# Kernel optimization log

Hardware: AMD Instinct MI355X
Metric: run time of the kernel (lower is better)

The kernel has to match this reference:

```python
import jax, jax.numpy as jnp
import numpy as np

B, S, V, K = 8, 128, 32000, 32


def setup_inputs() -> dict:
    key = jax.random.key(0)
    ks = jax.random.split(key, 8)
    return {
        "neural_logit": jax.random.normal(ks[0], (B, S, V), dtype=jnp.float32),
        "optor_vals": jax.random.randint(ks[1], (B, S, K), 0, V),
        "optor_dists": jax.random.uniform(ks[2], (B, S, K), dtype=jnp.float32) * 100.0,
        "const_vals": jax.random.randint(ks[3], (B, S, K), 0, V),
        "const_dists": jax.random.uniform(ks[4], (B, S, K), dtype=jnp.float32) * 100.0,
        "prev_words": jax.random.randint(ks[5], (B, S), 0, V),
        "optor_lamda": jnp.array([0.7], dtype=jnp.float32),
        "const_lamda": jnp.array([0.7], dtype=jnp.float32),
        "optor_temp": jnp.array([10.0], dtype=jnp.float32),
        "const_temp": jnp.array([10.0], dtype=jnp.float32),
    }


def _knn_prob(vals, dists, temp, vocab):
    # kernel-density: softmax over negative distances, scatter-add into vocab ids
    b, s, k = vals.shape
    w = jax.nn.softmax(-dists / temp, axis=-1)            # [B,S,K]
    rows = jnp.arange(b * s)[:, None]                     # [BS,1]
    p = jnp.zeros((b * s, vocab), w.dtype)
    p = p.at[rows, vals.reshape(b * s, k)].add(w.reshape(b * s, k))
    return p.reshape(b, s, vocab)


def reference(neural_logit, optor_vals, optor_dists, const_vals, const_dists,
              prev_words, optor_lamda, const_lamda, optor_temp, const_temp):
    nmt_prob = jax.nn.softmax(neural_logit, axis=-1)      # [B,S,V]

    optor_knn = _knn_prob(optor_vals, optor_dists, optor_temp[0], V)
    optor_combined = optor_lamda[0] * optor_knn + (1.0 - optor_lamda[0]) * nmt_prob

    const_knn = _knn_prob(const_vals, const_dists, const_temp[0], V)
    const_combined = const_lamda[0] * const_knn + (1.0 - const_lamda[0]) * nmt_prob

    pw = prev_words                                        # [B,S]
    optor_mask = (pw <= 88) | ((pw >= 91) & (pw <= 291))
    const_mask = (pw == 89) | (pw == 90) | (pw >= 292)

    combined = (optor_combined * optor_mask[:, :, None].astype(nmt_prob.dtype)
                + const_combined * const_mask[:, :, None].astype(nmt_prob.dtype))
    return combined
```

## Files before the change

### kernel.cpp

```cpp
#include <hip/hip_runtime.h>
#include <math.h>

constexpr int Bc = 8, Sc = 128, Vc = 32000, Kc = 32;
constexpr int NT = 1024;
constexpr int V4 = Vc / 4;
constexpr int ITERS = (V4 + NT - 1) / NT;
constexpr int NWAVES = NT / 64;

__global__ __launch_bounds__(NT) void SR_knnModel_kernel(
    const float* __restrict__ logit,
    const int*   __restrict__ optor_vals,
    const float* __restrict__ optor_dists,
    const int*   __restrict__ const_vals,
    const float* __restrict__ const_dists,
    const int*   __restrict__ prev_words,
    const float* __restrict__ optor_lamda,
    const float* __restrict__ const_lamda,
    const float* __restrict__ optor_temp,
    const float* __restrict__ const_temp,
    float* __restrict__ out)
{
    const int row = blockIdx.x;
    const int t   = threadIdx.x;
    const size_t base = (size_t)row * Vc;
    const float4* __restrict__ xin  = (const float4*)(logit + base);
    float4* __restrict__       xout = (float4*)(out + base);

    float4 r[ITERS];
    float lmax = -INFINITY;
#pragma unroll
    for (int i = 0; i < ITERS; ++i) {
        const int idx = t + i * NT;
        if (i < ITERS - 1 || idx < V4) {
            const float4 v = xin[idx];
            r[i] = v;
            lmax = fmaxf(lmax, fmaxf(fmaxf(v.x, v.y), fmaxf(v.z, v.w)));
        }
    }

    __shared__ float red[NWAVES];
#pragma unroll
    for (int off = 32; off > 0; off >>= 1)
        lmax = fmaxf(lmax, __shfl_xor(lmax, off));
    const int wave = t >> 6;
    if ((t & 63) == 0) red[wave] = lmax;
    __syncthreads();
    float bmax = red[0];
#pragma unroll
    for (int w = 1; w < NWAVES; ++w) bmax = fmaxf(bmax, red[w]);
    __syncthreads();

    float lsum = 0.f;
#pragma unroll
    for (int i = 0; i < ITERS; ++i) {
        const int idx = t + i * NT;
        if (i < ITERS - 1 || idx < V4) {
            float4 v = r[i];
            v.x = __expf(v.x - bmax);
            v.y = __expf(v.y - bmax);
            v.z = __expf(v.z - bmax);
            v.w = __expf(v.w - bmax);
            r[i] = v;
            lsum += (v.x + v.y) + (v.z + v.w);
        }
    }
#pragma unroll
    for (int off = 32; off > 0; off >>= 1)
        lsum += __shfl_xor(lsum, off);
    if ((t & 63) == 0) red[wave] = lsum;
    __syncthreads();
    float bsum = 0.f;
#pragma unroll
    for (int w = 0; w < NWAVES; ++w) bsum += red[w];

    const int pw = prev_words[row];
    const bool om = (pw <= 88) || (pw >= 91 && pw <= 291);
    const bool cm = (pw == 89) || (pw == 90) || (pw >= 292);
    const float omf = om ? 1.f : 0.f;
    const float cmf = cm ? 1.f : 0.f;
    const float ol = optor_lamda[0];
    const float cl = const_lamda[0];
    const float cn = (1.f - ol) * omf + (1.f - cl) * cmf;
    const float inv = cn / bsum;

#pragma unroll
    for (int i = 0; i < ITERS; ++i) {
        const int idx = t + i * NT;
        if (i < ITERS - 1 || idx < V4) {
            float4 v = r[i];
            v.x *= inv; v.y *= inv; v.z *= inv; v.w *= inv;
            xout[idx] = v;
        }
    }
    __syncthreads();

    if (t < 32 || (t >= 64 && t < 96)) {
        const bool is_opt = (t < 32);
        const float scale = is_opt ? ol * omf : cl * cmf;
        if (scale != 0.f) {
            const int k = t & 31;
            const int*   vals  = is_opt ? optor_vals  : const_vals;
            const float* dists = is_opt ? optor_dists : const_dists;
            const float  temp  = is_opt ? optor_temp[0] : const_temp[0];
            const float s = -dists[row * Kc + k] / temp;
            float m = s;
#pragma unroll
            for (int off = 16; off > 0; off >>= 1)
                m = fmaxf(m, __shfl_xor(m, off));
            const float e = __expf(s - m);
            float sm = e;
#pragma unroll
            for (int off = 16; off > 0; off >>= 1)
                sm += __shfl_xor(sm, off);
            const float w = e / sm;
            atomicAdd(out + base + vals[row * Kc + k], scale * w);
        }
    }
}

extern "C" void kernel_launch(void* const* d_in, const int* in_sizes, int n_in,
                              void* d_out, int out_size, void* d_ws, size_t ws_size,
                              hipStream_t stream) {
    const float* logit       = (const float*)d_in[0];
    const int*   optor_vals  = (const int*)  d_in[1];
    const float* optor_dists = (const float*)d_in[2];
    const int*   const_vals  = (const int*)  d_in[3];
    const float* const_dists = (const float*)d_in[4];
    const int*   prev_words  = (const int*)  d_in[5];
    const float* optor_lamda = (const float*)d_in[6];
    const float* const_lamda = (const float*)d_in[7];
    const float* optor_temp  = (const float*)d_in[8];
    const float* const_temp  = (const float*)d_in[9];
    float* out = (float*)d_out;

    SR_knnModel_kernel<<<Bc * Sc, NT, 0, stream>>>(
        logit, optor_vals, optor_dists, const_vals, const_dists, prev_words,
        optor_lamda, const_lamda, optor_temp, const_temp, out);
}
```

Measured before the change: 252.5 us.

## Use online softmax with a single merged max/sum reduction, halve block size

Replaces the two block-wide reductions (max, then sum) with one online-softmax reduction. Each thread exponentiates against its own local max, and (max, sum) pairs are merged across the wave and across waves with rescaling. This removes one reduction round and its barriers. The block size drops from 1024 to 512 threads with a hint of 6 blocks per CU, so each thread holds more float4 registers. That adds register pressure and a few extra exps per merge step.

```diff
diff --git a/kernel.cpp b/kernel.cpp
--- a/kernel.cpp
+++ b/kernel.cpp
@@ -2,12 +2,12 @@
 #include <math.h>
 
 constexpr int Bc = 8, Sc = 128, Vc = 32000, Kc = 32;
-constexpr int NT = 1024;
+constexpr int NT = 512;
 constexpr int V4 = Vc / 4;
 constexpr int ITERS = (V4 + NT - 1) / NT;
 constexpr int NWAVES = NT / 64;
 
-__global__ __launch_bounds__(NT) void SR_knnModel_kernel(
+__global__ __launch_bounds__(NT, 6) void SR_knnModel_kernel(
     const float* __restrict__ logit,
     const int*   __restrict__ optor_vals,
     const float* __restrict__ optor_dists,
@@ -38,57 +38,60 @@
         }
     }
 
-    __shared__ float red[NWAVES];
-#pragma unroll
-    for (int off = 32; off > 0; off >>= 1)
-        lmax = fmaxf(lmax, __shfl_xor(lmax, off));
-    const int wave = t >> 6;
-    if ((t & 63) == 0) red[wave] = lmax;
-    __syncthreads();
-    float bmax = red[0];
-#pragma unroll
-    for (int w = 1; w < NWAVES; ++w) bmax = fmaxf(bmax, red[w]);
-    __syncthreads();
-
     float lsum = 0.f;
 #pragma unroll
     for (int i = 0; i < ITERS; ++i) {
         const int idx = t + i * NT;
         if (i < ITERS - 1 || idx < V4) {
             float4 v = r[i];
-            v.x = __expf(v.x - bmax);
-            v.y = __expf(v.y - bmax);
-            v.z = __expf(v.z - bmax);
-            v.w = __expf(v.w - bmax);
+            v.x = __expf(v.x - lmax);
+            v.y = __expf(v.y - lmax);
+            v.z = __expf(v.z - lmax);
+            v.w = __expf(v.w - lmax);
             r[i] = v;
             lsum += (v.x + v.y) + (v.z + v.w);
         }
     }
-#pragma unroll
-    for (int off = 32; off > 0; off >>= 1)
-        lsum += __shfl_xor(lsum, off);
-    if ((t & 63) == 0) red[wave] = lsum;
-    __syncthreads();
-    float bsum = 0.f;
-#pragma unroll
-    for (int w = 0; w < NWAVES; ++w) bsum += red[w];
 
     const int pw = prev_words[row];
-    const bool om = (pw <= 88) || (pw >= 91 && pw <= 291);
-    const bool cm = (pw == 89) || (pw == 90) || (pw >= 292);
-    const float omf = om ? 1.f : 0.f;
-    const float cmf = cm ? 1.f : 0.f;
     const float ol = optor_lamda[0];
     const float cl = const_lamda[0];
+
+    float m = lmax, s = lsum;
+#pragma unroll
+    for (int off = 32; off > 0; off >>= 1) {
+        const float om = __shfl_xor(m, off);
+        const float os = __shfl_xor(s, off);
+        const float M  = fmaxf(m, om);
+        s = s * __expf(m - M) + os * __expf(om - M);
+        m = M;
+    }
+    __shared__ float2 red[NWAVES];
+    const int wave = t >> 6;
+    if ((t & 63) == 0) red[wave] = make_float2(m, s);
+    __syncthreads();
+    float M = red[0].x, S = red[0].y;
+#pragma unroll
+    for (int w = 1; w < NWAVES; ++w) {
+        const float2 p = red[w];
+        const float nM = fmaxf(M, p.x);
+        S = S * __expf(M - nM) + p.y * __expf(p.x - nM);
+        M = nM;
+    }
+
+    const bool om_ = (pw <= 88) || (pw >= 91 && pw <= 291);
+    const bool cm_ = (pw == 89) || (pw == 90) || (pw >= 292);
+    const float omf = om_ ? 1.f : 0.f;
+    const float cmf = cm_ ? 1.f : 0.f;
     const float cn = (1.f - ol) * omf + (1.f - cl) * cmf;
-    const float inv = cn / bsum;
+    const float f = __expf(lmax - M) * (cn / S);
 
 #pragma unroll
     for (int i = 0; i < ITERS; ++i) {
         const int idx = t + i * NT;
         if (i < ITERS - 1 || idx < V4) {
             float4 v = r[i];
-            v.x *= inv; v.y *= inv; v.z *= inv; v.w *= inv;
+            v.x *= f; v.y *= f; v.z *= f; v.w *= f;
             xout[idx] = v;
         }
     }
@@ -102,12 +105,12 @@
             const int*   vals  = is_opt ? optor_vals  : const_vals;
             const float* dists = is_opt ? optor_dists : const_dists;
             const float  temp  = is_opt ? optor_temp[0] : const_temp[0];
-            const float s = -dists[row * Kc + k] / temp;
-            float m = s;
+            const float sc = -dists[row * Kc + k] / temp;
+            float mm = sc;
 #pragma unroll
             for (int off = 16; off > 0; off >>= 1)
-                m = fmaxf(m, __shfl_xor(m, off));
-            const float e = __expf(s - m);
+                mm = fmaxf(mm, __shfl_xor(mm, off));
+            const float e = __expf(sc - mm);
             float sm = e;
 #pragma unroll
             for (int off = 16; off > 0; off >>= 1)
```

Measured after the change: 270.8 us. +7.3%, slower.
